# Kernel optimization log

Measured on AMD Instinct MI355X. Metric: run time of the kernel, lower is better.

Reference implementation:

```python
import jax, jax.numpy as jnp
import numpy as np

N, D_IN, D_OUT, E, K, H = 8192, 256, 256, 16, 2, 512


def setup_inputs() -> dict:
    key = jax.random.key(0)
    ks = jax.random.split(key, 11)
    return {
        "x": jax.random.normal(ks[0], (N, D_IN), jnp.float32),
        "gate_w": jax.random.normal(ks[1], (D_IN, H), jnp.float32),
        "gate_b": jax.random.normal(ks[2], (H,), jnp.float32),
        "gate_out_w": jax.random.normal(ks[3], (H, E), jnp.float32),
        "gate_out_b": jax.random.normal(ks[4], (E,), jnp.float32),
        "mlp_w1": jax.random.normal(ks[5], (D_IN, E, H), jnp.float32),
        "mlp_b1": jax.random.normal(ks[6], (E, H), jnp.float32),
        "mlp_w2": jax.random.normal(ks[7], (H, E, H), jnp.float32),
        "mlp_b2": jax.random.normal(ks[8], (E, H), jnp.float32),
        "mlp_w3": jax.random.normal(ks[9], (H, E, D_OUT), jnp.float32),
        "mlp_b3": jax.random.normal(ks[10], (E, D_OUT), jnp.float32),
    }


def reference(x, gate_w, gate_b, gate_out_w, gate_out_b,
              mlp_w1, mlp_b1, mlp_w2, mlp_b2, mlp_w3, mlp_b3):
    n, e = x.shape[0], gate_out_w.shape[1]
    # Gate MLP: relu(x @ Wg + bg) @ Wo + bo -> [N, E]
    logits = jax.nn.relu(x @ gate_w + gate_b) @ gate_out_w + gate_out_b
    # Top-k expert selection + softmax over selected gate values
    top_vals, top_idx = jax.lax.top_k(logits, K)              # [N, K]
    gates = jax.nn.softmax(top_vals, axis=-1)                 # [N, K]
    # Scatter into a sparse combine matrix [N, E] (top-k indices are unique per row)
    combine = jnp.zeros((n, e), x.dtype).at[jnp.arange(n)[:, None], top_idx].set(gates)
    # Per-expert 3-layer MLP, computed densely over all experts then combined.
    h1 = jax.nn.relu(jnp.einsum('ni,ieh->neh', x, mlp_w1) + mlp_b1)    # [N, E, H]
    h2 = jax.nn.relu(jnp.einsum('neh,heg->neg', h1, mlp_w2) + mlp_b2)  # [N, E, H]
    ye = jnp.einsum('neg,geo->neo', h2, mlp_w3) + mlp_b3               # [N, E, D_OUT]
    # Gate-weighted combine over experts (only top-k contribute)
    return jnp.einsum('neo,ne->no', ye, combine)
```

## Files before the change

kernel.cpp:

```cpp
#include <hip/hip_runtime.h>
#include <hip/hip_bf16.h>
#include <stdint.h>

#define NTOK 8192
#define DIN  256
#define DOUT 256
#define NEXP 16
#define HID  512
#define NKA  (NTOK*2)
#define NBLK (NTOK/256)
#define MAXTILE 272
#define GK 768

typedef __bf16 bf16x8 __attribute__((ext_vector_type(8)));
typedef __bf16 bf16x4 __attribute__((ext_vector_type(4)));
typedef float  f32x4  __attribute__((ext_vector_type(4)));

__device__ __forceinline__ void async_cp16(const __bf16* g, __bf16* l) {
  __builtin_amdgcn_global_load_lds(
      (const __attribute__((address_space(1))) unsigned int*)g,
      (__attribute__((address_space(3))) unsigned int*)l, 16, 0, 0);
}

__device__ __forceinline__ void transpose_cvt_body(const float* __restrict__ src,
                                                   __bf16* __restrict__ dst,
                                                   int K, int N, int bx, int by, int bz,
                                                   int tx, int ty, float (*t)[33]) {
  int e = bz, k0 = bx * 32, n0 = by * 32;
  #pragma unroll
  for (int j = 0; j < 4; j++) {
    int kl = ty + j * 8;
    t[kl][tx] = src[(size_t)(k0 + kl) * (NEXP * N) + (size_t)e * N + n0 + tx];
  }
  __syncthreads();
  #pragma unroll
  for (int j = 0; j < 4; j++) {
    int nl = ty + j * 8;
    dst[(size_t)e * N * K + (size_t)(n0 + nl) * K + k0 + tx] = (__bf16)t[tx][nl];
  }
}

__global__ __launch_bounds__(256) void prep_kernel(
    const float* __restrict__ x, __bf16* __restrict__ xs,
    const float* __restrict__ gw, __bf16* __restrict__ gwt,
    float* __restrict__ logitz) {
  __shared__ float t[32][33];
  int idx = blockIdx.x;
  int tid = threadIdx.x;
  int tx = tid & 31, ty = tid >> 5;
  if (idx < 2048) {
    int i = idx * 256 + tid;
    float4 v = ((const float4*)x)[i];
    int base = i * 4;
    int tk = base >> 8, c = base & 255;
    bf16x4 hi = { (__bf16)v.x, (__bf16)v.y, (__bf16)v.z, (__bf16)v.w };
    bf16x4 lo = { (__bf16)(v.x - (float)hi[0]), (__bf16)(v.y - (float)hi[1]),
                  (__bf16)(v.z - (float)hi[2]), (__bf16)(v.w - (float)hi[3]) };
    __bf16* row = xs + (size_t)tk * GK + c;
    *(bf16x4*)(row)       = hi;
    *(bf16x4*)(row + 256) = lo;
    *(bf16x4*)(row + 512) = hi;
  } else if (idx < 2176) {
    int g = idx - 2048;
    int k0 = (g & 7) * 32, n0 = (g >> 3) * 32;
    #pragma unroll
    for (int j = 0; j < 4; j++) {
      int kl = ty + j * 8;
      t[kl][tx] = gw[(size_t)(k0 + kl) * HID + n0 + tx];
    }
    __syncthreads();
    #pragma unroll
    for (int j = 0; j < 4; j++) {
      int nl = ty + j * 8;
      float v = t[tx][nl];
      __bf16 hi = (__bf16)v;
      __bf16 lo = (__bf16)(v - (float)hi);
      __bf16* drow = gwt + (size_t)(n0 + nl) * GK + k0 + tx;
      drow[0]   = hi;
      drow[256] = hi;
      drow[512] = lo;
    }
  } else {
    int i = (idx - 2176) * 256 + tid;
    ((float4*)logitz)[i] = make_float4(0.f, 0.f, 0.f, 0.f);
  }
}

__global__ __launch_bounds__(256) void gate_fused_kernel(
    const __bf16* __restrict__ xs, const __bf16* __restrict__ gwt,
    const float* __restrict__ gate_b, float* __restrict__ logits,
    const float* __restrict__ gow,
    const float* __restrict__ w1, __bf16* __restrict__ w1t,
    const float* __restrict__ w2, __bf16* __restrict__ w2t,
    const float* __restrict__ w3, __bf16* __restrict__ w3t) {
  __shared__ __align__(16) char smem[8192 + 64 * 132 * 4];
  int bx = blockIdx.x;
  int tid = threadIdx.x;

  if (bx >= 512) {
    float (*t)[33] = (float (*)[33])smem;
    int tx = tid & 31, ty = tid >> 5;
    int g = bx - 512;
    if (g < 2048) {
      transpose_cvt_body(w1, w1t, DIN, HID, g & 7, (g >> 3) & 15, g >> 7, tx, ty, t);
    } else if (g < 6144) {
      int g2 = g - 2048;
      transpose_cvt_body(w2, w2t, HID, HID, g2 & 15, (g2 >> 4) & 15, g2 >> 8, tx, ty, t);
    } else {
      int g3 = g - 6144;
      transpose_cvt_body(w3, w3t, HID, DOUT, g3 & 15, (g3 >> 4) & 7, g3 >> 7, tx, ty, t);
    }
    return;
  }

  int mt = bx >> 2, nt = bx & 3;
  __bf16* AlB = (__bf16*)smem;
  __bf16* BlB = (__bf16*)(smem + 8192);

  int lane = tid & 63, w = tid >> 6;
  int l16 = lane & 15, quad = lane >> 4;

  int r0 = tid >> 2;
  int q8 = ((tid & 3) ^ ((r0 >> 1) & 3)) * 8;
  const __bf16* apg  = xs + (size_t)(mt * 64 + r0) * GK + q8;
  const __bf16* bpg0 = gwt + (size_t)(nt * 128 + r0) * GK + q8;
  const __bf16* bpg1 = bpg0 + (size_t)64 * GK;

  __bf16* al0 = AlB;
  __bf16* al1 = AlB + 2048;
  __bf16* bl0 = BlB;
  __bf16* bl1 = BlB + 4096;

  f32x4 acc[4][2];
  #pragma unroll
  for (int i = 0; i < 4; i++)
    #pragma unroll
    for (int j = 0; j < 2; j++) acc[i][j] = {0.f, 0.f, 0.f, 0.f};

  async_cp16(apg, al0 + tid * 8);
  async_cp16(bpg0, bl0 + tid * 8);
  async_cp16(bpg1, bl0 + (tid + 256) * 8);

  int qs = (quad ^ ((l16 >> 1) & 3)) * 8;

  const int nIter = GK >> 5;
  for (int it = 0; it < nIter; ++it) {
    int buf = it & 1;
    if (it + 1 < nIter) {
      int kb = (it + 1) << 5;
      __bf16* an = buf ? al0 : al1;
      __bf16* bn = buf ? bl0 : bl1;
      async_cp16(apg + kb, an + tid * 8);
      async_cp16(bpg0 + kb, bn + tid * 8);
      async_cp16(bpg1 + kb, bn + (tid + 256) * 8);
      asm volatile("s_waitcnt vmcnt(3)" ::: "memory");
    } else {
      asm volatile("s_waitcnt vmcnt(0)" ::: "memory");
    }
    __builtin_amdgcn_s_barrier();
    asm volatile("" ::: "memory");
    const __bf16* ab = buf ? al1 : al0;
    const __bf16* bb = buf ? bl1 : bl0;
    bf16x8 af[4], bfr[2];
    #pragma unroll
    for (int i = 0; i < 4; i++)
      af[i] = *(const bf16x8*)(ab + (size_t)(i * 16 + l16) * 32 + qs);
    #pragma unroll
    for (int i = 0; i < 2; i++)
      bfr[i] = *(const bf16x8*)(bb + (size_t)(w * 32 + i * 16 + l16) * 32 + qs);
    #pragma unroll
    for (int mi = 0; mi < 4; mi++)
      #pragma unroll
      for (int ni = 0; ni < 2; ni++)
        acc[mi][ni] = __builtin_amdgcn_mfma_f32_16x16x32_bf16(af[mi], bfr[ni], acc[mi][ni], 0, 0, 0);
    asm volatile("" ::: "memory");
    __builtin_amdgcn_s_barrier();
  }

  __syncthreads();
  float* wl = (float*)smem;
  float* ht = (float*)(smem + 8192);
  if (tid < 128) {
    const float* gr = gow + (size_t)(nt * 128 + tid) * 16;
    #pragma unroll
    for (int j = 0; j < 4; j++)
      *(float4*)&wl[tid * 16 + j * 4] = *(const float4*)&gr[j * 4];
  }
  float bv[2];
  #pragma unroll
  for (int ni = 0; ni < 2; ni++) bv[ni] = gate_b[nt * 128 + w * 32 + ni * 16 + l16];
  #pragma unroll
  for (int mi = 0; mi < 4; mi++)
    #pragma unroll
    for (int ni = 0; ni < 2; ni++)
      #pragma unroll
      for (int r = 0; r < 4; r++) {
        int row = mi * 16 + quad * 4 + r;
        int col = w * 32 + ni * 16 + l16;
        ht[row * 132 + col] = fmaxf(acc[mi][ni][r] + bv[ni], 0.f);
      }
  __syncthreads();
  int t = tid >> 2, e4 = (tid & 3) * 4;
  float s0 = 0.f, s1 = 0.f, s2 = 0.f, s3 = 0.f;
  #pragma unroll 4
  for (int h = 0; h < 128; h++) {
    float hv = ht[t * 132 + h];
    const float* wr = &wl[h * 16 + e4];
    s0 = fmaf(hv, wr[0], s0);
    s1 = fmaf(hv, wr[1], s1);
    s2 = fmaf(hv, wr[2], s2);
    s3 = fmaf(hv, wr[3], s3);
  }
  float* lp = logits + (size_t)(mt * 64 + t) * 16 + e4;
  atomicAdd(lp + 0, s0);
  atomicAdd(lp + 1, s1);
  atomicAdd(lp + 2, s2);
  atomicAdd(lp + 3, s3);
}

__global__ __launch_bounds__(256) void top2_kernel(const float* __restrict__ logits,
                                                   const float* __restrict__ gb,
                                                   int2* __restrict__ e01,
                                                   float2* __restrict__ g01,
                                                   int* __restrict__ lrank,
                                                   int* __restrict__ blockhist) {
  __shared__ int hist[NEXP];
  __shared__ float gbl[NEXP];
  int tid = threadIdx.x;
  if (tid < NEXP) { hist[tid] = 0; gbl[tid] = gb[tid]; }
  __syncthreads();
  int t = blockIdx.x * 256 + tid;
  float lv[16];
  const float4* lp = (const float4*)(logits + (size_t)t * 16);
  #pragma unroll
  for (int j = 0; j < 4; j++) {
    float4 v = lp[j];
    lv[4*j]   = v.x + gbl[4*j];
    lv[4*j+1] = v.y + gbl[4*j+1];
    lv[4*j+2] = v.z + gbl[4*j+2];
    lv[4*j+3] = v.w + gbl[4*j+3];
  }
  float v0 = -3.402823466e38f, v1 = -3.402823466e38f;
  int i0 = 0, i1 = 0;
  #pragma unroll
  for (int e = 0; e < 16; e++) {
    float v = lv[e];
    if (v > v0) { v1 = v0; i1 = i0; v0 = v; i0 = e; }
    else if (v > v1) { v1 = v; i1 = e; }
  }
  float ew = expf(v1 - v0);
  float inv = 1.f / (1.f + ew);
  e01[t] = make_int2(i0, i1);
  g01[t] = make_float2(inv, ew * inv);
  int r0 = atomicAdd(&hist[i0], 1);
  int r1 = atomicAdd(&hist[i1], 1);
  lrank[2 * t]     = r0;
  lrank[2 * t + 1] = r1;
  __syncthreads();
  if (tid < NEXP) blockhist[blockIdx.x * NEXP + tid] = hist[tid];
}

__global__ __launch_bounds__(256) void fillscan_kernel(const int2* __restrict__ e01,
                                                       const int* __restrict__ lrank,
                                                       const int* __restrict__ blockhist,
                                                       int* __restrict__ tok_sorted,
                                                       int* __restrict__ route_pos,
                                                       int* __restrict__ offsets,
                                                       int* __restrict__ tile_e,
                                                       int* __restrict__ tile_mt,
                                                       int* __restrict__ ntiles) {
  __shared__ int tot_s[NEXP], pre_s[NEXP], soff[NEXP + 1], base_l[NEXP], tbase[NEXP];
  int b = blockIdx.x;
  int tid = threadIdx.x;
  if (tid < NEXP) {
    int s_all = 0, s_pre = 0;
    for (int bb = 0; bb < NBLK; bb++) {
      int h = blockhist[bb * NEXP + tid];
      s_pre += (bb < b) ? h : 0;
      s_all += h;
    }
    tot_s[tid] = s_all;
    pre_s[tid] = s_pre;
  }
  __syncthreads();
  if (tid == 0) {
    int s = 0, tb = 0;
    for (int i = 0; i < NEXP; i++) {
      soff[i] = s; s += tot_s[i];
      tbase[i] = tb; tb += (tot_s[i] + 63) >> 6;
    }
    soff[NEXP] = s;
    if (b == 0) *ntiles = tb;
  }
  __syncthreads();
  if (tid < NEXP) base_l[tid] = soff[tid] + pre_s[tid];
  if (b == 0) {
    if (tid < NEXP + 1) offsets[tid] = soff[tid];
    if (tid < NEXP) {
      int nt = (tot_s[tid] + 63) >> 6, tb0 = tbase[tid];
      for (int m = 0; m < nt; m++) { tile_e[tb0 + m] = tid; tile_mt[tb0 + m] = m; }
    }
  }
  __syncthreads();
  int t = b * 256 + tid;
  int2 e = e01[t];
  int p0 = base_l[e.x] + lrank[2 * t];
  int p1 = base_l[e.y] + lrank[2 * t + 1];
  tok_sorted[p0] = t; route_pos[2 * t]     = p0;
  tok_sorted[p1] = t; route_pos[2 * t + 1] = p1;
}

template<bool RELU>
__global__ __launch_bounds__(256) void moe_gemm_kernel(const __bf16* __restrict__ A,
                                                       const __bf16* __restrict__ Bt,
                                                       const float* __restrict__ bias,
                                                       __bf16* __restrict__ out,
                                                       const int* __restrict__ seg_off,
                                                       const int* __restrict__ gather,
                                                       const int* __restrict__ tile_e,
                                                       const int* __restrict__ tile_mt,
                                                       const int* __restrict__ ntiles,
                                                       int LDA, int K, int N) {
  int bx = blockIdx.x;
  if (bx >= *ntiles) return;
  int e  = tile_e[bx];
  int mt = tile_mt[bx];
  int off = seg_off[e];
  int Te  = seg_off[e + 1] - off;
  int nt = blockIdx.y;

  __shared__ __align__(16) char smem[24576];
  __bf16* AlB = (__bf16*)smem;
  __bf16* BlB = (__bf16*)(smem + 8192);

  int tid = threadIdx.x;
  int lane = tid & 63, w = tid >> 6;
  int l16 = lane & 15, quad = lane >> 4;

  int r0 = tid >> 2;
  int q8 = ((tid & 3) ^ ((r0 >> 1) & 3)) * 8;
  int rowA = mt * 64 + r0;
  int rA = rowA < Te ? rowA : Te - 1;
  size_t ga = gather ? (size_t)gather[off + rA] : (size_t)(off + rA);
  const __bf16* apg  = A + ga * LDA + q8;
  const __bf16* Bte  = Bt + (size_t)e * N * K;
  const __bf16* bpg0 = Bte + (size_t)(nt * 128 + r0) * K + q8;
  const __bf16* bpg1 = bpg0 + (size_t)64 * K;

  __bf16* al0 = AlB;
  __bf16* al1 = AlB + 2048;
  __bf16* bl0 = BlB;
  __bf16* bl1 = BlB + 4096;

  f32x4 acc[4][2];
  #pragma unroll
  for (int i = 0; i < 4; i++)
    #pragma unroll
    for (int j = 0; j < 2; j++) acc[i][j] = {0.f, 0.f, 0.f, 0.f};

  async_cp16(apg, al0 + tid * 8);
  async_cp16(bpg0, bl0 + tid * 8);
  async_cp16(bpg1, bl0 + (tid + 256) * 8);

  int qs = (quad ^ ((l16 >> 1) & 3)) * 8;

  int nIter = K >> 5;
  for (int it = 0; it < nIter; ++it) {
    int buf = it & 1;
    if (it + 1 < nIter) {
      int kb = (it + 1) << 5;
      __bf16* an = buf ? al0 : al1;
      __bf16* bn = buf ? bl0 : bl1;
      async_cp16(apg + kb, an + tid * 8);
      async_cp16(bpg0 + kb, bn + tid * 8);
      async_cp16(bpg1 + kb, bn + (tid + 256) * 8);
      asm volatile("s_waitcnt vmcnt(3)" ::: "memory");
    } else {
      asm volatile("s_waitcnt vmcnt(0)" ::: "memory");
    }
    __builtin_amdgcn_s_barrier();
    asm volatile("" ::: "memory");
    const __bf16* ab = buf ? al1 : al0;
    const __bf16* bb = buf ? bl1 : bl0;
    bf16x8 af[4], bfr[2];
    #pragma unroll
    for (int i = 0; i < 4; i++)
      af[i] = *(const bf16x8*)(ab + (size_t)(i * 16 + l16) * 32 + qs);
    #pragma unroll
    for (int i = 0; i < 2; i++)
      bfr[i] = *(const bf16x8*)(bb + (size_t)(w * 32 + i * 16 + l16) * 32 + qs);
    #pragma unroll
    for (int mi = 0; mi < 4; mi++)
      #pragma unroll
      for (int ni = 0; ni < 2; ni++)
        acc[mi][ni] = __builtin_amdgcn_mfma_f32_16x16x32_bf16(af[mi], bfr[ni], acc[mi][ni], 0, 0, 0);
    asm volatile("" ::: "memory");
    __builtin_amdgcn_s_barrier();
  }

  const float* be = bias + (size_t)e * N;
  #pragma unroll
  for (int ni = 0; ni < 2; ni++) {
    int col = nt * 128 + w * 32 + ni * 16 + l16;
    float bv = be[col];
    #pragma unroll
    for (int mi = 0; mi < 4; mi++) {
      #pragma unroll
      for (int r = 0; r < 4; r++) {
        int row_in = mt * 64 + mi * 16 + quad * 4 + r;
        if (row_in < Te) {
          float v = acc[mi][ni][r] + bv;
          if (RELU) v = fmaxf(v, 0.f);
          out[(size_t)(off + row_in) * N + col] = (__bf16)v;
        }
      }
    }
  }
}

__global__ void combine_kernel(const __bf16* __restrict__ Y, const int* __restrict__ route_pos,
                               const float2* __restrict__ g01, float* __restrict__ out) {
  int gid = blockIdx.x * blockDim.x + threadIdx.x;
  int t = gid >> 6, c = (gid & 63) << 2;
  if (t >= NTOK) return;
  int p0 = route_pos[2 * t], p1 = route_pos[2 * t + 1];
  float2 g = g01[t];
  bf16x4 y0 = *(const bf16x4*)&Y[(size_t)p0 * DOUT + c];
  bf16x4 y1 = *(const bf16x4*)&Y[(size_t)p1 * DOUT + c];
  float4 o;
  o.x = g.x * (float)y0[0] + g.y * (float)y1[0];
  o.y = g.x * (float)y0[1] + g.y * (float)y1[1];
  o.z = g.x * (float)y0[2] + g.y * (float)y1[2];
  o.w = g.x * (float)y0[3] + g.y * (float)y1[3];
  *(float4*)&out[(size_t)t * DOUT + c] = o;
}

extern "C" void kernel_launch(void* const* d_in, const int* in_sizes, int n_in,
                              void* d_out, int out_size, void* d_ws, size_t ws_size,
                              hipStream_t stream) {
  const float* x          = (const float*)d_in[0];
  const float* gate_w     = (const float*)d_in[1];
  const float* gate_b     = (const float*)d_in[2];
  const float* gate_out_w = (const float*)d_in[3];
  const float* gate_out_b = (const float*)d_in[4];
  const float* w1         = (const float*)d_in[5];
  const float* b1         = (const float*)d_in[6];
  const float* w2         = (const float*)d_in[7];
  const float* b2         = (const float*)d_in[8];
  const float* w3         = (const float*)d_in[9];
  const float* b3         = (const float*)d_in[10];
  float* out = (float*)d_out;

  char* ws = (char*)d_ws;
  size_t o = 0;
  auto alloc = [&](size_t bytes) -> void* {
    o = (o + 255) & ~(size_t)255;
    void* p = ws + o;
    o += bytes;
    return p;
  };

  __bf16* w1t  = (__bf16*)alloc((size_t)NEXP * HID * DIN * 2);
  __bf16* w2t  = (__bf16*)alloc((size_t)NEXP * HID * HID * 2);
  __bf16* w3t  = (__bf16*)alloc((size_t)NEXP * DOUT * HID * 2);
  __bf16* gwt  = (__bf16*)alloc((size_t)HID * GK * 2);
  __bf16* H1   = (__bf16*)alloc((size_t)(NKA + 128) * HID * 2);
  size_t r3 = (size_t)NTOK * GK * 2;
  size_t r4 = (size_t)(NKA + 128) * HID * 2;
  void* region2 = alloc(r3 > r4 ? r3 : r4);
  __bf16* xs = (__bf16*)region2;
  __bf16* H2 = (__bf16*)region2;
  float* logits    = (float*)alloc((size_t)NTOK * 16 * 4);
  int2*  e01       = (int2*)alloc((size_t)NTOK * 8);
  float2* g01      = (float2*)alloc((size_t)NTOK * 8);
  int*   offsets   = (int*)alloc((NEXP + 1) * 4);
  int*   blockhist = (int*)alloc((size_t)NBLK * NEXP * 4);
  int*   lrank     = (int*)alloc((size_t)NTOK * 2 * 4);
  int*   tok_sorted= (int*)alloc((size_t)(NKA + 128) * 4);
  int*   route_pos = (int*)alloc((size_t)NTOK * 2 * 4);
  int*   tile_e    = (int*)alloc(MAXTILE * 4);
  int*   tile_mt   = (int*)alloc(MAXTILE * 4);
  int*   ntiles    = (int*)alloc(4);
  __bf16* Y        = (__bf16*)alloc((size_t)(NKA + 128) * DOUT * 2);
  (void)ws_size; (void)n_in; (void)in_sizes; (void)out_size;

  prep_kernel<<<2304, 256, 0, stream>>>(x, xs, gate_w, gwt, logits);

  gate_fused_kernel<<<8704, 256, 0, stream>>>(xs, gwt, gate_b, logits, gate_out_w,
                                              w1, w1t, w2, w2t, w3, w3t);

  top2_kernel<<<NBLK, 256, 0, stream>>>(logits, gate_out_b, e01, g01, lrank, blockhist);
  fillscan_kernel<<<NBLK, 256, 0, stream>>>(e01, lrank, blockhist, tok_sorted, route_pos,
                                            offsets, tile_e, tile_mt, ntiles);

  moe_gemm_kernel<true><<<dim3(MAXTILE, HID / 128), 256, 0, stream>>>(
      xs, w1t, b1, H1, offsets, tok_sorted, tile_e, tile_mt, ntiles, GK, DIN, HID);
  moe_gemm_kernel<true><<<dim3(MAXTILE, HID / 128), 256, 0, stream>>>(
      H1, w2t, b2, H2, offsets, nullptr, tile_e, tile_mt, ntiles, HID, HID, HID);
  moe_gemm_kernel<false><<<dim3(MAXTILE, DOUT / 128), 256, 0, stream>>>(
      H2, w3t, b3, Y, offsets, nullptr, tile_e, tile_mt, ntiles, HID, HID, DOUT);

  combine_kernel<<<(NTOK * 64) / 256, 256, 0, stream>>>(Y, route_pos, g01, out);
}
```

Measured before the change: 201.2 us.

## Double GEMM K-step to 64 and remap tile order across blocks

```diff
diff --git a/kernel.cpp b/kernel.cpp
--- a/kernel.cpp
+++ b/kernel.cpp
@@ -321,7 +321,8 @@
                                                        const int* __restrict__ tile_mt,
                                                        const int* __restrict__ ntiles,
                                                        int LDA, int K, int N) {
-  int bx = blockIdx.x;
+  int bx0 = blockIdx.x;
+  int bx = (bx0 & 7) * (MAXTILE >> 3) + (bx0 >> 3);
   if (bx >= *ntiles) return;
   int e  = tile_e[bx];
   int mt = tile_mt[bx];
@@ -329,28 +330,34 @@
   int Te  = seg_off[e + 1] - off;
   int nt = blockIdx.y;
 
-  __shared__ __align__(16) char smem[24576];
+  __shared__ __align__(16) char smem[49152];
   __bf16* AlB = (__bf16*)smem;
-  __bf16* BlB = (__bf16*)(smem + 8192);
+  __bf16* BlB = (__bf16*)(smem + 16384);
 
   int tid = threadIdx.x;
   int lane = tid & 63, w = tid >> 6;
   int l16 = lane & 15, quad = lane >> 4;
 
-  int r0 = tid >> 2;
-  int q8 = ((tid & 3) ^ ((r0 >> 1) & 3)) * 8;
-  int rowA = mt * 64 + r0;
-  int rA = rowA < Te ? rowA : Te - 1;
-  size_t ga = gather ? (size_t)gather[off + rA] : (size_t)(off + rA);
-  const __bf16* apg  = A + ga * LDA + q8;
+  int r0 = tid >> 3;
+  int q8 = ((tid & 7) ^ (r0 & 7)) * 8;
+  int rowA0 = mt * 64 + r0;
+  int rowA1 = rowA0 + 32;
+  int rA0 = rowA0 < Te ? rowA0 : Te - 1;
+  int rA1 = rowA1 < Te ? rowA1 : Te - 1;
+  size_t ga0 = gather ? (size_t)gather[off + rA0] : (size_t)(off + rA0);
+  size_t ga1 = gather ? (size_t)gather[off + rA1] : (size_t)(off + rA1);
+  const __bf16* apg0 = A + ga0 * LDA + q8;
+  const __bf16* apg1 = A + ga1 * LDA + q8;
   const __bf16* Bte  = Bt + (size_t)e * N * K;
   const __bf16* bpg0 = Bte + (size_t)(nt * 128 + r0) * K + q8;
-  const __bf16* bpg1 = bpg0 + (size_t)64 * K;
+  const __bf16* bpg1 = bpg0 + (size_t)32 * K;
+  const __bf16* bpg2 = bpg0 + (size_t)64 * K;
+  const __bf16* bpg3 = bpg0 + (size_t)96 * K;
 
   __bf16* al0 = AlB;
-  __bf16* al1 = AlB + 2048;
+  __bf16* al1 = AlB + 4096;
   __bf16* bl0 = BlB;
-  __bf16* bl1 = BlB + 4096;
+  __bf16* bl1 = BlB + 8192;
 
   f32x4 acc[4][2];
   #pragma unroll
@@ -358,23 +365,29 @@
     #pragma unroll
     for (int j = 0; j < 2; j++) acc[i][j] = {0.f, 0.f, 0.f, 0.f};
 
-  async_cp16(apg, al0 + tid * 8);
+  async_cp16(apg0, al0 + tid * 8);
+  async_cp16(apg1, al0 + (tid + 256) * 8);
   async_cp16(bpg0, bl0 + tid * 8);
   async_cp16(bpg1, bl0 + (tid + 256) * 8);
-
-  int qs = (quad ^ ((l16 >> 1) & 3)) * 8;
-
-  int nIter = K >> 5;
+  async_cp16(bpg2, bl0 + (tid + 512) * 8);
+  async_cp16(bpg3, bl0 + (tid + 768) * 8);
+
+  int x7 = (l16 & 7);
+
+  int nIter = K >> 6;
   for (int it = 0; it < nIter; ++it) {
     int buf = it & 1;
     if (it + 1 < nIter) {
-      int kb = (it + 1) << 5;
+      int kb = (it + 1) << 6;
       __bf16* an = buf ? al0 : al1;
       __bf16* bn = buf ? bl0 : bl1;
-      async_cp16(apg + kb, an + tid * 8);
+      async_cp16(apg0 + kb, an + tid * 8);
+      async_cp16(apg1 + kb, an + (tid + 256) * 8);
       async_cp16(bpg0 + kb, bn + tid * 8);
       async_cp16(bpg1 + kb, bn + (tid + 256) * 8);
-      asm volatile("s_waitcnt vmcnt(3)" ::: "memory");
+      async_cp16(bpg2 + kb, bn + (tid + 512) * 8);
+      async_cp16(bpg3 + kb, bn + (tid + 768) * 8);
+      asm volatile("s_waitcnt vmcnt(6)" ::: "memory");
     } else {
       asm volatile("s_waitcnt vmcnt(0)" ::: "memory");
     }
@@ -382,18 +395,22 @@
     asm volatile("" ::: "memory");
     const __bf16* ab = buf ? al1 : al0;
     const __bf16* bb = buf ? bl1 : bl0;
-    bf16x8 af[4], bfr[2];
-    #pragma unroll
-    for (int i = 0; i < 4; i++)
-      af[i] = *(const bf16x8*)(ab + (size_t)(i * 16 + l16) * 32 + qs);
-    #pragma unroll
-    for (int i = 0; i < 2; i++)
-      bfr[i] = *(const bf16x8*)(bb + (size_t)(w * 32 + i * 16 + l16) * 32 + qs);
-    #pragma unroll
-    for (int mi = 0; mi < 4; mi++)
+    #pragma unroll
+    for (int kk = 0; kk < 2; kk++) {
+      int qs = ((kk * 4 + quad) ^ x7) * 8;
+      bf16x8 af[4], bfr[2];
       #pragma unroll
-      for (int ni = 0; ni < 2; ni++)
-        acc[mi][ni] = __builtin_amdgcn_mfma_f32_16x16x32_bf16(af[mi], bfr[ni], acc[mi][ni], 0, 0, 0);
+      for (int i = 0; i < 4; i++)
+        af[i] = *(const bf16x8*)(ab + (size_t)(i * 16 + l16) * 64 + qs);
+      #pragma unroll
+      for (int i = 0; i < 2; i++)
+        bfr[i] = *(const bf16x8*)(bb + (size_t)(w * 32 + i * 16 + l16) * 64 + qs);
+      #pragma unroll
+      for (int mi = 0; mi < 4; mi++)
+        #pragma unroll
+        for (int ni = 0; ni < 2; ni++)
+          acc[mi][ni] = __builtin_amdgcn_mfma_f32_16x16x32_bf16(af[mi], bfr[ni], acc[mi][ni], 0, 0, 0);
+    }
     asm volatile("" ::: "memory");
     __builtin_amdgcn_s_barrier();
   }
```

Result: faster. 193.9 us (-3.6%).
